# Kernel tuning notes

Hardware: AMD Instinct MI355X
Metric: run time of the kernel (lower is better)

## Reference

```python
import jax, jax.numpy as jnp
import numpy as np

D, H, DH, L, F, NM = 512, 8, 64, 8, 2048, 80
B, S = 8, 1024


def _ln(x, g, b, eps=1e-5):
    mu = x.mean(-1, keepdims=True)
    var = ((x - mu) ** 2).mean(-1, keepdims=True)
    return (x - mu) / jnp.sqrt(var + eps) * g + b


def setup_inputs() -> dict:
    key = jax.random.key(0)
    ks = jax.random.split(key, 16)
    n = lambda k, sh: jax.random.normal(k, sh, dtype=jnp.float32) * 0.02
    # sinusoidal positional encoding, as in PositionalEncoding
    pos = np.arange(S, dtype=np.float32)[:, None]
    div = np.exp(np.arange(0, D, 2, dtype=np.float32) * (-np.log(10000.0) / D))
    pe = np.zeros((S, D), dtype=np.float32)
    pe[:, 0::2] = np.sin(pos * div)
    pe[:, 1::2] = np.cos(pos * div)
    return dict(
        mel=jax.random.normal(ks[0], (B, S, NM), dtype=jnp.float32),
        pe=jnp.asarray(pe),
        proj_w=n(ks[1], (NM, D)), proj_b=jnp.zeros((D,), jnp.float32),
        Wq=n(ks[2], (L, D, D)), bq=jnp.zeros((L, D), jnp.float32),
        Wk=n(ks[3], (L, D, D)), bk=jnp.zeros((L, D), jnp.float32),
        Wv=n(ks[4], (L, D, D)), bv=jnp.zeros((L, D), jnp.float32),
        Wo=n(ks[5], (L, D, D)), bo=jnp.zeros((L, D), jnp.float32),
        ln1_g=jnp.ones((L, D), jnp.float32), ln1_b=jnp.zeros((L, D), jnp.float32),
        ln2_g=jnp.ones((L, D), jnp.float32), ln2_b=jnp.zeros((L, D), jnp.float32),
        Wi=n(ks[6], (L, D, F)), bi=jnp.zeros((L, F), jnp.float32),
        Wf=n(ks[7], (L, F, D)), bf=jnp.zeros((L, D), jnp.float32),
        lnf_g=jnp.ones((D,), jnp.float32), lnf_b=jnp.zeros((D,), jnp.float32),
        lang_w=n(ks[8], (D, 100)), lang_b=jnp.zeros((100,), jnp.float32),
        int_w=n(ks[9], (D, 50)), int_b=jnp.zeros((50,), jnp.float32),
        emo_w=n(ks[10], (D, 8)), emo_b=jnp.zeros((8,), jnp.float32),
        sp_w=n(ks[11], (D, 1000)), sp_b=jnp.zeros((1000,), jnp.float32),
    )


def reference(mel, pe, proj_w, proj_b, Wq, bq, Wk, bk, Wv, bv, Wo, bo,
              ln1_g, ln1_b, ln2_g, ln2_b, Wi, bi, Wf, bf,
              lnf_g, lnf_b, lang_w, lang_b, int_w, int_b, emo_w, emo_b, sp_w, sp_b):
    # feature extraction projection + positional encoding
    h = mel @ proj_w + proj_b + pe[None]  # (B, S, D)
    scale = 1.0 / np.sqrt(DH)

    def block(h, p):
        wq, bq_, wk, bk_, wv, bv_, wo, bo_, g1, b1, g2, b2, wi, bi_, wf, bf_ = p
        x = _ln(h, g1, b1)
        b, s, _ = x.shape
        heads = lambda y, w, bias: (y @ w + bias).reshape(b, s, H, DH).transpose(0, 2, 1, 3)
        q, k, v = heads(x, wq, bq_), heads(x, wk, bk_), heads(x, wv, bv_)
        probs = jax.nn.softmax(jnp.einsum('bhqd,bhkd->bhqk', q, k) * scale, axis=-1)
        ctx = jnp.einsum('bhqk,bhkd->bhqd', probs, v).transpose(0, 2, 1, 3).reshape(b, s, D)
        h = h + ctx @ wo + bo_
        y = _ln(h, g2, b2)
        h = h + jax.nn.gelu(y @ wi + bi_, approximate=False) @ wf + bf_
        return h, None

    h, _ = jax.lax.scan(block, h, (Wq, bq, Wk, bk, Wv, bv, Wo, bo,
                                   ln1_g, ln1_b, ln2_g, ln2_b, Wi, bi, Wf, bf))
    h = _ln(h, lnf_g, lnf_b)
    pooled = h.mean(axis=1)  # no mask: sequence_lengths=None path
    language_logits = pooled @ lang_w + lang_b
    intent_logits = pooled @ int_w + int_b
    emotion_logits = pooled @ emo_w + emo_b
    speech_logits = h @ sp_w + sp_b
    return (language_logits, intent_logits, emotion_logits, speech_logits)
```

## Files before the change

### kernel.cpp

```cpp
#include <hip/hip_runtime.h>
#include <hip/hip_bf16.h>
#include <math.h>

#define DD   512
#define HH   8
#define DHH  64
#define LL   8
#define FF   2048
#define NMEL 80
#define BB   8
#define SS   1024
#define MM   (BB*SS)

typedef __attribute__((ext_vector_type(8))) short bf16x8;
typedef __attribute__((ext_vector_type(4))) float f32x4;
typedef __attribute__((ext_vector_type(4))) unsigned short u16x4;

#define GLOAD_LDS16(g, l) __builtin_amdgcn_global_load_lds( \
    (const __attribute__((address_space(1))) void*)(g),      \
    (__attribute__((address_space(3))) void*)(l), 16, 0, 0)

__device__ __forceinline__ unsigned short f2bf(float x) {
    __hip_bfloat16 b = __float2bfloat16(x);
    return *reinterpret_cast<unsigned short*>(&b);
}

__global__ __launch_bounds__(256) void proj_pe_kernel(
    const float* __restrict__ mel, const float* __restrict__ pw,
    const float* __restrict__ pb, const float* __restrict__ pe,
    float* __restrict__ h)
{
    int row = blockIdx.x;
    int s = row & (SS - 1);
    __shared__ float m_s[NMEL];
    int t = threadIdx.x;
    if (t < NMEL) m_s[t] = mel[(size_t)row * NMEL + t];
    __syncthreads();
    for (int d = t; d < DD; d += 256) {
        float acc = pb[d] + pe[(size_t)s * DD + d];
        #pragma unroll 8
        for (int k = 0; k < NMEL; ++k)
            acc = fmaf(m_s[k], pw[(size_t)k * DD + d], acc);
        h[(size_t)row * DD + d] = acc;
    }
}

__global__ __launch_bounds__(256) void ln_kernel(
    const float* __restrict__ in, const float* __restrict__ g,
    const float* __restrict__ bta, __hip_bfloat16* __restrict__ out)
{
    int row = blockIdx.x;
    const float* xr = in + (size_t)row * DD;
    int t = threadIdx.x;
    float x0 = xr[t], x1 = xr[t + 256];
    float s = x0 + x1;
    float ss = x0 * x0 + x1 * x1;
    #pragma unroll
    for (int off = 32; off; off >>= 1) {
        s  += __shfl_down(s, off);
        ss += __shfl_down(ss, off);
    }
    __shared__ float red1[4], red2[4];
    int lane = t & 63, w = t >> 6;
    if (lane == 0) { red1[w] = s; red2[w] = ss; }
    __syncthreads();
    s  = red1[0] + red1[1] + red1[2] + red1[3];
    ss = red2[0] + red2[1] + red2[2] + red2[3];
    float mu  = s * (1.f / DD);
    float var = ss * (1.f / DD) - mu * mu;
    float rstd = rsqrtf(var + 1e-5f);
    out[(size_t)row * DD + t]       = __float2bfloat16((x0 - mu) * rstd * g[t]       + bta[t]);
    out[(size_t)row * DD + t + 256] = __float2bfloat16((x1 - mu) * rstd * g[t + 256] + bta[t + 256]);
}

__global__ __launch_bounds__(256) void wconv_kernel(
    const float* __restrict__ in, __hip_bfloat16* __restrict__ out,
    int K, int N, int rstride, int rowoff)
{
    __shared__ float tile[32][33];
    size_t lin  = (size_t)blockIdx.z * K * N;
    size_t lout = (size_t)blockIdx.z * rstride * K + (size_t)rowoff * K;
    int tx = threadIdx.x & 31, ty = threadIdx.x >> 5;
    int n0 = blockIdx.x * 32, k0 = blockIdx.y * 32;
    #pragma unroll
    for (int i = 0; i < 32; i += 8) {
        int k = k0 + ty + i, n = n0 + tx;
        tile[ty + i][tx] = (n < N) ? in[lin + (size_t)k * N + n] : 0.f;
    }
    __syncthreads();
    #pragma unroll
    for (int i = 0; i < 32; i += 8) {
        int n = n0 + ty + i, k = k0 + tx;
        out[lout + (size_t)n * K + k] = __float2bfloat16(tile[tx][ty + i]);
    }
}

template<int OUTMODE, bool GELU_EP, bool RESID>
__global__ __launch_bounds__(512) void gemm_bf16(
    const __hip_bfloat16* __restrict__ A,
    const __hip_bfloat16* __restrict__ Bt,
    const float* __restrict__ b0, const float* __restrict__ b1,
    const float* __restrict__ b2,
    const float* __restrict__ resid,
    float* __restrict__ Cf,
    __hip_bfloat16* __restrict__ O0, __hip_bfloat16* __restrict__ O1,
    __hip_bfloat16* __restrict__ O2,
    int M, int N, int K)
{
    __shared__ __align__(16) __hip_bfloat16 As[128 * 64];
    __shared__ __align__(16) __hip_bfloat16 Bs[128 * 64];
    int t = threadIdx.x;
    int w = t >> 6, lane = t & 63, g = lane >> 4, li = lane & 15;
    int wm = w >> 2, wn = w & 3;
    size_t bm = (size_t)blockIdx.y * 128;
    size_t bn = (size_t)blockIdx.x * 128;

    const f32x4 vzero = {0.f, 0.f, 0.f, 0.f};
    f32x4 acc[4][2];
    #pragma unroll
    for (int i = 0; i < 4; ++i)
        #pragma unroll
        for (int j = 0; j < 2; ++j) acc[i][j] = vzero;

    for (int k0 = 0; k0 < K; k0 += 64) {
        #pragma unroll
        for (int i = 0; i < 2; ++i) {
            int c = i * 512 + t;
            int row = c >> 3, col = (c & 7) << 3;
            GLOAD_LDS16(A + (bm + row) * (size_t)K + k0 + col, As + (size_t)c * 8);
        }
        #pragma unroll
        for (int i = 0; i < 2; ++i) {
            int c = i * 512 + t;
            int row = c >> 3, col = (c & 7) << 3;
            GLOAD_LDS16(Bt + (bn + row) * (size_t)K + k0 + col, Bs + (size_t)c * 8);
        }
        __syncthreads();
        #pragma unroll
        for (int kk = 0; kk < 2; ++kk) {
            bf16x8 af[4], bfr[2];
            #pragma unroll
            for (int mi = 0; mi < 4; ++mi)
                af[mi] = *reinterpret_cast<const bf16x8*>(As + (wm * 64 + mi * 16 + li) * 64 + kk * 32 + g * 8);
            #pragma unroll
            for (int ni = 0; ni < 2; ++ni)
                bfr[ni] = *reinterpret_cast<const bf16x8*>(Bs + (wn * 32 + ni * 16 + li) * 64 + kk * 32 + g * 8);
            #pragma unroll
            for (int mi = 0; mi < 4; ++mi)
                #pragma unroll
                for (int ni = 0; ni < 2; ++ni)
                    acc[mi][ni] = __builtin_amdgcn_mfma_f32_16x16x32_bf16(af[mi], bfr[ni], acc[mi][ni], 0, 0, 0);
        }
        __syncthreads();
    }

    #pragma unroll
    for (int mi = 0; mi < 4; ++mi) {
        #pragma unroll
        for (int ni = 0; ni < 2; ++ni) {
            f32x4 v = acc[mi][ni];
            int coll = wn * 32 + ni * 16 + li;
            size_t col = bn + coll;
            if ((int)col >= N) continue;
            float bv;
            int sel = 0, c = (int)col;
            if (OUTMODE == 2) {
                sel = (int)(col >> 9); c = (int)(col & 511);
                bv = (sel == 0) ? b0[c] : (sel == 1) ? b1[c] : b2[c];
            } else {
                bv = b0[col];
            }
            #pragma unroll
            for (int r = 0; r < 4; ++r) {
                size_t row = bm + wm * 64 + mi * 16 + g * 4 + r;
                float x = v[r] + bv;
                if (GELU_EP) x = 0.5f * x * (1.f + erff(x * 0.70710678118654752440f));
                if (RESID)   x += resid[row * (size_t)N + col];
                if (OUTMODE == 0) {
                    Cf[row * (size_t)N + col] = x;
                } else if (OUTMODE == 1) {
                    O0[row * (size_t)N + col] = __float2bfloat16(x);
                } else {
                    size_t b = row >> 10, s = row & (SS - 1);
                    size_t h = (size_t)(c >> 6), d = (size_t)(c & 63);
                    __hip_bfloat16 xb = __float2bfloat16(x);
                    if (sel == 0)      O0[((b * HH + h) << 16) + (s << 6) + d] = xb;
                    else if (sel == 1) O1[((b * HH + h) << 16) + (s << 6) + d] = xb;
                    else               O2[((b * HH + h) << 16) + (d << 10) + s] = xb;
                }
            }
        }
    }
}

__global__ __launch_bounds__(512, 4) void attn_mfma(
    const __hip_bfloat16* __restrict__ qb,
    const __hip_bfloat16* __restrict__ kb,
    const __hip_bfloat16* __restrict__ vtb,
    __hip_bfloat16* __restrict__ ctx)
{
    __shared__ __align__(16) char smem[49152];
    unsigned short (*Plds)[32][40] = (unsigned short (*)[32][40])smem;
    float* comb = (float*)smem;

    int t = threadIdx.x;
    int w = t >> 6, lane = t & 63, g = lane >> 4, li = lane & 15;
    int wq = w & 3, wk = w >> 2;
    int bh = blockIdx.y;
    int b = bh >> 3, h = bh & 7;
    int q0 = blockIdx.x * 128 + wq * 32;

    const __hip_bfloat16* Qp = qb  + ((size_t)bh << 16);
    const __hip_bfloat16* Kp = kb  + ((size_t)bh << 16);
    const __hip_bfloat16* Vp = vtb + ((size_t)bh << 16);

    bf16x8 qf[2][2];
    #pragma unroll
    for (int qt = 0; qt < 2; ++qt)
        #pragma unroll
        for (int kk = 0; kk < 2; ++kk)
            qf[qt][kk] = *reinterpret_cast<const bf16x8*>(
                Qp + (size_t)(q0 + qt * 16 + li) * DHH + kk * 32 + g * 8);

    const f32x4 vzero = {0.f, 0.f, 0.f, 0.f};
    f32x4 acc_oT[2][4];
    float m_r[2], l_r[2];
    #pragma unroll
    for (int qt = 0; qt < 2; ++qt) {
        #pragma unroll
        for (int dt = 0; dt < 4; ++dt) acc_oT[qt][dt] = vzero;
        m_r[qt] = -1e30f; l_r[qt] = 0.f;
    }

    const float csc = 0.125f * 1.44269504088896340736f;

    for (int it = 0; it < 16; ++it) {
        int ks0 = wk * 512 + it * 32;
        f32x4 accs[2][2];
        #pragma unroll
        for (int qt = 0; qt < 2; ++qt)
            #pragma unroll
            for (int kt = 0; kt < 2; ++kt) accs[qt][kt] = vzero;
        #pragma unroll
        for (int kk = 0; kk < 2; ++kk) {
            bf16x8 kf[2];
            #pragma unroll
            for (int kt = 0; kt < 2; ++kt)
                kf[kt] = *reinterpret_cast<const bf16x8*>(
                    Kp + (size_t)(ks0 + kt * 16 + li) * DHH + kk * 32 + g * 8);
            #pragma unroll
            for (int qt = 0; qt < 2; ++qt)
                #pragma unroll
                for (int kt = 0; kt < 2; ++kt)
                    accs[qt][kt] = __builtin_amdgcn_mfma_f32_16x16x32_bf16(kf[kt], qf[qt][kk], accs[qt][kt], 0, 0, 0);
        }

        float mnew[2];
        #pragma unroll
        for (int qt = 0; qt < 2; ++qt) {
            float a0 = fmaxf(fmaxf(accs[qt][0][0], accs[qt][0][1]),
                             fmaxf(accs[qt][0][2], accs[qt][0][3]));
            float a1 = fmaxf(fmaxf(accs[qt][1][0], accs[qt][1][1]),
                             fmaxf(accs[qt][1][2], accs[qt][1][3]));
            float m = fmaxf(a0, a1);
            m = fmaxf(m, __shfl_xor(m, 16));
            m = fmaxf(m, __shfl_xor(m, 32));
            mnew[qt] = m * csc;
        }

        bool grow = (mnew[0] > m_r[0] + 11.0f) || (mnew[1] > m_r[1] + 11.0f);
        if (__any(grow)) {
            #pragma unroll
            for (int qt = 0; qt < 2; ++qt) {
                float mn = fmaxf(m_r[qt], mnew[qt]);
                float alpha = exp2f(m_r[qt] - mn);
                m_r[qt] = mn;
                l_r[qt] *= alpha;
                #pragma unroll
                for (int dt = 0; dt < 4; ++dt)
                    #pragma unroll
                    for (int r = 0; r < 4; ++r)
                        acc_oT[qt][dt][r] *= alpha;
            }
        }

        float rs[2] = {0.f, 0.f};
        #pragma unroll
        for (int qt = 0; qt < 2; ++qt) {
            #pragma unroll
            for (int kt = 0; kt < 2; ++kt) {
                u16x4 pk;
                #pragma unroll
                for (int r = 0; r < 4; ++r) {
                    float p = exp2f(fmaf(accs[qt][kt][r], csc, -m_r[qt]));
                    rs[qt] += p;
                    pk[r] = f2bf(p);
                }
                *reinterpret_cast<u16x4*>(&Plds[w][qt * 16 + li][kt * 16 + g * 4]) = pk;
            }
            float s = rs[qt];
            s += __shfl_xor(s, 16);
            s += __shfl_xor(s, 32);
            l_r[qt] += s;
        }

        __builtin_amdgcn_wave_barrier();

        bf16x8 pf[2];
        #pragma unroll
        for (int qt = 0; qt < 2; ++qt)
            pf[qt] = *reinterpret_cast<const bf16x8*>(&Plds[w][qt * 16 + li][g * 8]);
        #pragma unroll
        for (int dt = 0; dt < 4; ++dt) {
            bf16x8 vf = *reinterpret_cast<const bf16x8*>(
                Vp + (size_t)(dt * 16 + li) * SS + ks0 + g * 8);
            #pragma unroll
            for (int qt = 0; qt < 2; ++qt)
                acc_oT[qt][dt] = __builtin_amdgcn_mfma_f32_16x16x32_bf16(vf, pf[qt], acc_oT[qt][dt], 0, 0, 0);
        }
        __builtin_amdgcn_wave_barrier();
    }

    __syncthreads();
    if (wk == 1) {
        float* cb = comb + ((size_t)(w - 4) * 64 + lane) * 36;
        #pragma unroll
        for (int qt = 0; qt < 2; ++qt)
            #pragma unroll
            for (int dt = 0; dt < 4; ++dt)
                *reinterpret_cast<f32x4*>(cb + qt * 16 + dt * 4) = acc_oT[qt][dt];
        #pragma unroll
        for (int qt = 0; qt < 2; ++qt) {
            cb[32 + qt] = m_r[qt];
            cb[34 + qt] = l_r[qt];
        }
    }
    __syncthreads();
    if (wk == 0) {
        float* cb = comb + ((size_t)w * 64 + lane) * 36;
        #pragma unroll
        for (int qt = 0; qt < 2; ++qt) {
            float m2 = cb[32 + qt];
            float l2 = cb[34 + qt];
            float mg = fmaxf(m_r[qt], m2);
            float a1 = exp2f(m_r[qt] - mg);
            float a2 = exp2f(m2 - mg);
            float inv = 1.f / (l_r[qt] * a1 + l2 * a2);
            int q = q0 + qt * 16 + li;
            #pragma unroll
            for (int dt = 0; dt < 4; ++dt) {
                f32x4 ob = *reinterpret_cast<const f32x4*>(cb + qt * 16 + dt * 4);
                u16x4 pk;
                #pragma unroll
                for (int r = 0; r < 4; ++r)
                    pk[r] = f2bf((acc_oT[qt][dt][r] * a1 + ob[r] * a2) * inv);
                *reinterpret_cast<u16x4*>(
                    &ctx[((size_t)(b * SS + q)) * DD + h * DHH + dt * 16 + g * 4]) = pk;
            }
        }
    }
}

__global__ __launch_bounds__(512) void pool_kernel(
    const __hip_bfloat16* __restrict__ hf, float* __restrict__ pooled)
{
    int b = blockIdx.x;
    int d = threadIdx.x;
    float acc = 0.f;
    for (int s = 0; s < SS; ++s)
        acc += __bfloat162float(hf[((size_t)(b * SS + s)) * DD + d]);
    pooled[b * DD + d] = acc * (1.f / SS);
}

__global__ __launch_bounds__(256) void heads_kernel(
    const float* __restrict__ pooled,
    const float* __restrict__ lw, const float* __restrict__ lb,
    const float* __restrict__ iw, const float* __restrict__ ib,
    const float* __restrict__ ew, const float* __restrict__ eb,
    float* __restrict__ out)
{
    int b = blockIdx.x;
    __shared__ float ps[DD];
    int t = threadIdx.x;
    ps[t] = pooled[b * DD + t];
    ps[t + 256] = pooled[b * DD + t + 256];
    __syncthreads();
    if (t < 158) {
        const float* wptr; const float* bptr; float* optr; int n; int j;
        if (t < 100)      { j = t;       wptr = lw; bptr = lb; optr = out;        n = 100; }
        else if (t < 150) { j = t - 100; wptr = iw; bptr = ib; optr = out + 800;  n = 50;  }
        else              { j = t - 150; wptr = ew; bptr = eb; optr = out + 1200; n = 8;   }
        float acc = bptr[j];
        for (int k2 = 0; k2 < DD; ++k2)
            acc = fmaf(ps[k2], wptr[(size_t)k2 * n + j], acc);
        optr[b * n + j] = acc;
    }
}

extern "C" void kernel_launch(void* const* d_in, const int* in_sizes, int n_in,
                              void* d_out, int out_size, void* d_ws, size_t ws_size,
                              hipStream_t stream)
{
    const float* mel    = (const float*)d_in[0];
    const float* pe     = (const float*)d_in[1];
    const float* proj_w = (const float*)d_in[2];
    const float* proj_b = (const float*)d_in[3];
    const float* Wq     = (const float*)d_in[4];
    const float* bq     = (const float*)d_in[5];
    const float* Wk     = (const float*)d_in[6];
    const float* bk     = (const float*)d_in[7];
    const float* Wv     = (const float*)d_in[8];
    const float* bv     = (const float*)d_in[9];
    const float* Wo     = (const float*)d_in[10];
    const float* bo     = (const float*)d_in[11];
    const float* ln1_g  = (const float*)d_in[12];
    const float* ln1_b  = (const float*)d_in[13];
    const float* ln2_g  = (const float*)d_in[14];
    const float* ln2_b  = (const float*)d_in[15];
    const float* Wi     = (const float*)d_in[16];
    const float* bi     = (const float*)d_in[17];
    const float* Wf     = (const float*)d_in[18];
    const float* bf     = (const float*)d_in[19];
    const float* lnf_g  = (const float*)d_in[20];
    const float* lnf_b  = (const float*)d_in[21];
    const float* lang_w = (const float*)d_in[22];
    const float* lang_b = (const float*)d_in[23];
    const float* int_w  = (const float*)d_in[24];
    const float* int_b  = (const float*)d_in[25];
    const float* emo_w  = (const float*)d_in[26];
    const float* emo_b  = (const float*)d_in[27];
    const float* sp_w   = (const float*)d_in[28];
    const float* sp_b   = (const float*)d_in[29];

    float* out = (float*)d_out;
    char* wsb = (char*)d_ws;

    const size_t MB = 1ull << 20;
    float* hbuf           = (float*)(wsb);
    __hip_bfloat16* xb    = (__hip_bfloat16*)(wsb + 16 * MB);
    __hip_bfloat16* qbuf  = (__hip_bfloat16*)(wsb + 24 * MB);
    __hip_bfloat16* kbuf  = (__hip_bfloat16*)(wsb + 32 * MB);
    __hip_bfloat16* vtb   = (__hip_bfloat16*)(wsb + 40 * MB);
    __hip_bfloat16* ctx   = (__hip_bfloat16*)(wsb + 48 * MB);
    __hip_bfloat16* gbuf  = (__hip_bfloat16*)(wsb + 24 * MB);
    float* pooled         = (float*)(wsb + 56 * MB);
    __hip_bfloat16* wqkv  = (__hip_bfloat16*)(wsb + 57 * MB);
    __hip_bfloat16* wot   = (__hip_bfloat16*)(wsb + 70 * MB);
    __hip_bfloat16* wit   = (__hip_bfloat16*)(wsb + 74 * MB);
    __hip_bfloat16* wft   = (__hip_bfloat16*)(wsb + 90 * MB);
    __hip_bfloat16* spt   = (__hip_bfloat16*)(wsb + 107 * MB);

    wconv_kernel<<<dim3(16, 16, LL), 256, 0, stream>>>(Wq, wqkv, DD, DD, 1536, 0);
    wconv_kernel<<<dim3(16, 16, LL), 256, 0, stream>>>(Wk, wqkv, DD, DD, 1536, 512);
    wconv_kernel<<<dim3(16, 16, LL), 256, 0, stream>>>(Wv, wqkv, DD, DD, 1536, 1024);
    wconv_kernel<<<dim3(16, 16, LL), 256, 0, stream>>>(Wo, wot, DD, DD, DD, 0);
    wconv_kernel<<<dim3(64, 16, LL), 256, 0, stream>>>(Wi, wit, DD, FF, FF, 0);
    wconv_kernel<<<dim3(16, 64, LL), 256, 0, stream>>>(Wf, wft, FF, DD, DD, 0);
    wconv_kernel<<<dim3(32, 16, 1),  256, 0, stream>>>(sp_w, spt, DD, 1000, 1024, 0);

    proj_pe_kernel<<<MM, 256, 0, stream>>>(mel, proj_w, proj_b, pe, hbuf);

    dim3 g512(4, 64);

    for (int l = 0; l < LL; ++l) {
        const __hip_bfloat16* wqkv_l = wqkv + (size_t)l * 1536 * DD;
        const __hip_bfloat16* wot_l  = wot  + (size_t)l * DD * DD;
        const __hip_bfloat16* wit_l  = wit  + (size_t)l * FF * DD;
        const __hip_bfloat16* wft_l  = wft  + (size_t)l * DD * FF;

        ln_kernel<<<MM, 256, 0, stream>>>(hbuf, ln1_g + l * DD, ln1_b + l * DD, xb);

        gemm_bf16<2, false, false><<<dim3(12, 64), 512, 0, stream>>>(
            xb, wqkv_l, bq + l * DD, bk + l * DD, bv + l * DD,
            nullptr, nullptr, qbuf, kbuf, vtb, MM, 1536, DD);

        attn_mfma<<<dim3(SS / 128, BB * HH), 512, 0, stream>>>(qbuf, kbuf, vtb, ctx);

        gemm_bf16<0, false, true><<<g512, 512, 0, stream>>>(
            ctx, wot_l, bo + l * DD, nullptr, nullptr,
            hbuf, hbuf, nullptr, nullptr, nullptr, MM, DD, DD);

        ln_kernel<<<MM, 256, 0, stream>>>(hbuf, ln2_g + l * DD, ln2_b + l * DD, xb);

        gemm_bf16<1, true, false><<<dim3(16, 64), 512, 0, stream>>>(
            xb, wit_l, bi + l * FF, nullptr, nullptr,
            nullptr, nullptr, gbuf, nullptr, nullptr, MM, FF, DD);
        gemm_bf16<0, false, true><<<g512, 512, 0, stream>>>(
            gbuf, wft_l, bf + l * DD, nullptr, nullptr,
            hbuf, hbuf, nullptr, nullptr, nullptr, MM, DD, FF);
    }

    ln_kernel<<<MM, 256, 0, stream>>>(hbuf, lnf_g, lnf_b, xb);
    pool_kernel<<<BB, 512, 0, stream>>>(xb, pooled);
    heads_kernel<<<BB, 256, 0, stream>>>(pooled, lang_w, lang_b, int_w, int_b,
                                         emo_w, emo_b, out);

    gemm_bf16<0, false, false><<<dim3(8, 64), 512, 0, stream>>>(
        xb, spt, sp_b, nullptr, nullptr,
        nullptr, out + 1264, nullptr, nullptr, nullptr, MM, 1000, DD);
}
```

Measured before the change: 1.885 ms.

## Use wave-per-row vectorized LayerNorm and 4-way key-split attention with larger key tiles

LayerNorm now processes one row per wavefront, eight rows per block, with float4 loads, xor-shuffle reductions and 16-byte bf16 stores, replacing the block-wide LDS reduction and barrier. The attention kernel now splits keys across four waves per query group (64 queries per block instead of 128) and processes 64 keys per iteration. That doubles the blocks and gives more MFMA work per softmax step. Partial results are merged in a two-level tree through shared memory, which adds extra barriers and LDS traffic at the end. The grid is also transposed so that heads vary fastest.

```diff
diff --git a/kernel.cpp b/kernel.cpp
--- a/kernel.cpp
+++ b/kernel.cpp
@@ -15,6 +15,7 @@
 typedef __attribute__((ext_vector_type(8))) short bf16x8;
 typedef __attribute__((ext_vector_type(4))) float f32x4;
 typedef __attribute__((ext_vector_type(4))) unsigned short u16x4;
+typedef __attribute__((ext_vector_type(8))) unsigned short u16x8;
 
 #define GLOAD_LDS16(g, l) __builtin_amdgcn_global_load_lds( \
     (const __attribute__((address_space(1))) void*)(g),      \
@@ -45,32 +46,38 @@
     }
 }
 
-__global__ __launch_bounds__(256) void ln_kernel(
+__global__ __launch_bounds__(512) void ln_kernel(
     const float* __restrict__ in, const float* __restrict__ g,
     const float* __restrict__ bta, __hip_bfloat16* __restrict__ out)
 {
-    int row = blockIdx.x;
-    const float* xr = in + (size_t)row * DD;
-    int t = threadIdx.x;
-    float x0 = xr[t], x1 = xr[t + 256];
-    float s = x0 + x1;
-    float ss = x0 * x0 + x1 * x1;
-    #pragma unroll
-    for (int off = 32; off; off >>= 1) {
-        s  += __shfl_down(s, off);
-        ss += __shfl_down(ss, off);
-    }
-    __shared__ float red1[4], red2[4];
-    int lane = t & 63, w = t >> 6;
-    if (lane == 0) { red1[w] = s; red2[w] = ss; }
-    __syncthreads();
-    s  = red1[0] + red1[1] + red1[2] + red1[3];
-    ss = red2[0] + red2[1] + red2[2] + red2[3];
+    int w = threadIdx.x >> 6, lane = threadIdx.x & 63;
+    int row = blockIdx.x * 8 + w;
+    const float4* xr = reinterpret_cast<const float4*>(in + (size_t)row * DD) + lane * 2;
+    float4 v0 = xr[0], v1 = xr[1];
+    float s  = v0.x + v0.y + v0.z + v0.w + v1.x + v1.y + v1.z + v1.w;
+    float ss = v0.x*v0.x + v0.y*v0.y + v0.z*v0.z + v0.w*v0.w
+             + v1.x*v1.x + v1.y*v1.y + v1.z*v1.z + v1.w*v1.w;
+    #pragma unroll
+    for (int off = 1; off < 64; off <<= 1) {
+        s  += __shfl_xor(s, off);
+        ss += __shfl_xor(ss, off);
+    }
     float mu  = s * (1.f / DD);
     float var = ss * (1.f / DD) - mu * mu;
     float rstd = rsqrtf(var + 1e-5f);
-    out[(size_t)row * DD + t]       = __float2bfloat16((x0 - mu) * rstd * g[t]       + bta[t]);
-    out[(size_t)row * DD + t + 256] = __float2bfloat16((x1 - mu) * rstd * g[t + 256] + bta[t + 256]);
+    const float4* gp = reinterpret_cast<const float4*>(g) + lane * 2;
+    const float4* bp = reinterpret_cast<const float4*>(bta) + lane * 2;
+    float4 g0 = gp[0], g1 = gp[1], b0 = bp[0], b1 = bp[1];
+    u16x8 o;
+    o[0] = f2bf((v0.x - mu) * rstd * g0.x + b0.x);
+    o[1] = f2bf((v0.y - mu) * rstd * g0.y + b0.y);
+    o[2] = f2bf((v0.z - mu) * rstd * g0.z + b0.z);
+    o[3] = f2bf((v0.w - mu) * rstd * g0.w + b0.w);
+    o[4] = f2bf((v1.x - mu) * rstd * g1.x + b1.x);
+    o[5] = f2bf((v1.y - mu) * rstd * g1.y + b1.y);
+    o[6] = f2bf((v1.z - mu) * rstd * g1.z + b1.z);
+    o[7] = f2bf((v1.w - mu) * rstd * g1.w + b1.w);
+    *reinterpret_cast<u16x8*>(out + (size_t)row * DD + lane * 8) = o;
 }
 
 __global__ __launch_bounds__(256) void wconv_kernel(
@@ -199,16 +206,16 @@
     const __hip_bfloat16* __restrict__ vtb,
     __hip_bfloat16* __restrict__ ctx)
 {
-    __shared__ __align__(16) char smem[49152];
-    unsigned short (*Plds)[32][40] = (unsigned short (*)[32][40])smem;
+    __shared__ __align__(16) char smem[36864];
+    unsigned short (*Plds)[32][72] = (unsigned short (*)[32][72])smem;
     float* comb = (float*)smem;
 
     int t = threadIdx.x;
     int w = t >> 6, lane = t & 63, g = lane >> 4, li = lane & 15;
-    int wq = w & 3, wk = w >> 2;
-    int bh = blockIdx.y;
+    int wq = w & 1, wk = w >> 1;
+    int bh = blockIdx.x;
     int b = bh >> 3, h = bh & 7;
-    int q0 = blockIdx.x * 128 + wq * 32;
+    int q0 = blockIdx.y * 64 + wq * 32;
 
     const __hip_bfloat16* Qp = qb  + ((size_t)bh << 16);
     const __hip_bfloat16* Kp = kb  + ((size_t)bh << 16);
@@ -234,35 +241,39 @@
 
     const float csc = 0.125f * 1.44269504088896340736f;
 
-    for (int it = 0; it < 16; ++it) {
-        int ks0 = wk * 512 + it * 32;
-        f32x4 accs[2][2];
+    for (int it = 0; it < 4; ++it) {
+        int ks0 = wk * 256 + it * 64;
+        f32x4 accs[2][4];
         #pragma unroll
         for (int qt = 0; qt < 2; ++qt)
             #pragma unroll
-            for (int kt = 0; kt < 2; ++kt) accs[qt][kt] = vzero;
+            for (int kt = 0; kt < 4; ++kt) accs[qt][kt] = vzero;
         #pragma unroll
         for (int kk = 0; kk < 2; ++kk) {
-            bf16x8 kf[2];
-            #pragma unroll
-            for (int kt = 0; kt < 2; ++kt)
+            bf16x8 kf[4];
+            #pragma unroll
+            for (int kt = 0; kt < 4; ++kt)
                 kf[kt] = *reinterpret_cast<const bf16x8*>(
                     Kp + (size_t)(ks0 + kt * 16 + li) * DHH + kk * 32 + g * 8);
             #pragma unroll
             for (int qt = 0; qt < 2; ++qt)
                 #pragma unroll
-                for (int kt = 0; kt < 2; ++kt)
+                for (int kt = 0; kt < 4; ++kt)
                     accs[qt][kt] = __builtin_amdgcn_mfma_f32_16x16x32_bf16(kf[kt], qf[qt][kk], accs[qt][kt], 0, 0, 0);
         }
 
         float mnew[2];
         #pragma unroll
         for (int qt = 0; qt < 2; ++qt) {
-            float a0 = fmaxf(fmaxf(accs[qt][0][0], accs[qt][0][1]),
-                             fmaxf(accs[qt][0][2], accs[qt][0][3]));
-            float a1 = fmaxf(fmaxf(accs[qt][1][0], accs[qt][1][1]),
-                             fmaxf(accs[qt][1][2], accs[qt][1][3]));
-            float m = fmaxf(a0, a1);
+            float m01 = fmaxf(fmaxf(accs[qt][0][0], accs[qt][0][1]),
+                              fmaxf(accs[qt][0][2], accs[qt][0][3]));
+            float m23 = fmaxf(fmaxf(accs[qt][1][0], accs[qt][1][1]),
+                              fmaxf(accs[qt][1][2], accs[qt][1][3]));
+            float m45 = fmaxf(fmaxf(accs[qt][2][0], accs[qt][2][1]),
+                              fmaxf(accs[qt][2][2], accs[qt][2][3]));
+            float m67 = fmaxf(fmaxf(accs[qt][3][0], accs[qt][3][1]),
+                              fmaxf(accs[qt][3][2], accs[qt][3][3]));
+            float m = fmaxf(fmaxf(m01, m23), fmaxf(m45, m67));
             m = fmaxf(m, __shfl_xor(m, 16));
             m = fmaxf(m, __shfl_xor(m, 32));
             mnew[qt] = m * csc;
@@ -284,64 +295,98 @@
             }
         }
 
-        float rs[2] = {0.f, 0.f};
         #pragma unroll
         for (int qt = 0; qt < 2; ++qt) {
-            #pragma unroll
-            for (int kt = 0; kt < 2; ++kt) {
+            float rs = 0.f;
+            #pragma unroll
+            for (int kt = 0; kt < 4; ++kt) {
                 u16x4 pk;
                 #pragma unroll
                 for (int r = 0; r < 4; ++r) {
                     float p = exp2f(fmaf(accs[qt][kt][r], csc, -m_r[qt]));
-                    rs[qt] += p;
+                    rs += p;
                     pk[r] = f2bf(p);
                 }
                 *reinterpret_cast<u16x4*>(&Plds[w][qt * 16 + li][kt * 16 + g * 4]) = pk;
             }
-            float s = rs[qt];
-            s += __shfl_xor(s, 16);
-            s += __shfl_xor(s, 32);
-            l_r[qt] += s;
+            rs += __shfl_xor(rs, 16);
+            rs += __shfl_xor(rs, 32);
+            l_r[qt] += rs;
         }
 
         __builtin_amdgcn_wave_barrier();
 
-        bf16x8 pf[2];
+        bf16x8 pf[2][2];
         #pragma unroll
         for (int qt = 0; qt < 2; ++qt)
-            pf[qt] = *reinterpret_cast<const bf16x8*>(&Plds[w][qt * 16 + li][g * 8]);
-        #pragma unroll
-        for (int dt = 0; dt < 4; ++dt) {
-            bf16x8 vf = *reinterpret_cast<const bf16x8*>(
-                Vp + (size_t)(dt * 16 + li) * SS + ks0 + g * 8);
-            #pragma unroll
-            for (int qt = 0; qt < 2; ++qt)
-                acc_oT[qt][dt] = __builtin_amdgcn_mfma_f32_16x16x32_bf16(vf, pf[qt], acc_oT[qt][dt], 0, 0, 0);
+            #pragma unroll
+            for (int ks = 0; ks < 2; ++ks)
+                pf[qt][ks] = *reinterpret_cast<const bf16x8*>(
+                    &Plds[w][qt * 16 + li][ks * 32 + g * 8]);
+        #pragma unroll
+        for (int ks = 0; ks < 2; ++ks) {
+            #pragma unroll
+            for (int dt = 0; dt < 4; ++dt) {
+                bf16x8 vf = *reinterpret_cast<const bf16x8*>(
+                    Vp + (size_t)(dt * 16 + li) * SS + ks0 + ks * 32 + g * 8);
+                #pragma unroll
+                for (int qt = 0; qt < 2; ++qt)
+                    acc_oT[qt][dt] = __builtin_amdgcn_mfma_f32_16x16x32_bf16(vf, pf[qt][ks], acc_oT[qt][dt], 0, 0, 0);
+            }
         }
         __builtin_amdgcn_wave_barrier();
     }
 
     __syncthreads();
-    if (wk == 1) {
-        float* cb = comb + ((size_t)(w - 4) * 64 + lane) * 36;
+    if (wk & 1) {
+        int slot = wq + (wk >> 1) * 2;
+        float* cb = comb + ((size_t)slot * 64 + lane) * 36;
         #pragma unroll
         for (int qt = 0; qt < 2; ++qt)
             #pragma unroll
             for (int dt = 0; dt < 4; ++dt)
                 *reinterpret_cast<f32x4*>(cb + qt * 16 + dt * 4) = acc_oT[qt][dt];
+        cb[32] = m_r[0]; cb[33] = m_r[1];
+        cb[34] = l_r[0]; cb[35] = l_r[1];
+    }
+    __syncthreads();
+    if (!(wk & 1)) {
+        int slot = wq + wk;
+        float* cb = comb + ((size_t)slot * 64 + lane) * 36;
         #pragma unroll
         for (int qt = 0; qt < 2; ++qt) {
-            cb[32 + qt] = m_r[qt];
-            cb[34 + qt] = l_r[qt];
-        }
+            float m2 = cb[32 + qt], l2 = cb[34 + qt];
+            float mg = fmaxf(m_r[qt], m2);
+            float a1 = exp2f(m_r[qt] - mg);
+            float a2 = exp2f(m2 - mg);
+            m_r[qt] = mg;
+            l_r[qt] = l_r[qt] * a1 + l2 * a2;
+            #pragma unroll
+            for (int dt = 0; dt < 4; ++dt) {
+                f32x4 ob = *reinterpret_cast<const f32x4*>(cb + qt * 16 + dt * 4);
+                #pragma unroll
+                for (int r = 0; r < 4; ++r)
+                    acc_oT[qt][dt][r] = acc_oT[qt][dt][r] * a1 + ob[r] * a2;
+            }
+        }
+    }
+    __syncthreads();
+    if (wk == 2) {
+        float* cb = comb + ((size_t)wq * 64 + lane) * 36;
+        #pragma unroll
+        for (int qt = 0; qt < 2; ++qt)
+            #pragma unroll
+            for (int dt = 0; dt < 4; ++dt)
+                *reinterpret_cast<f32x4*>(cb + qt * 16 + dt * 4) = acc_oT[qt][dt];
+        cb[32] = m_r[0]; cb[33] = m_r[1];
+        cb[34] = l_r[0]; cb[35] = l_r[1];
     }
     __syncthreads();
     if (wk == 0) {
-        float* cb = comb + ((size_t)w * 64 + lane) * 36;
+        float* cb = comb + ((size_t)wq * 64 + lane) * 36;
         #pragma unroll
         for (int qt = 0; qt < 2; ++qt) {
-            float m2 = cb[32 + qt];
-            float l2 = cb[34 + qt];
+            float m2 = cb[32 + qt], l2 = cb[34 + qt];
             float mg = fmaxf(m_r[qt], m2);
             float a1 = exp2f(m_r[qt] - mg);
             float a2 = exp2f(m2 - mg);
@@ -468,19 +513,19 @@
         const __hip_bfloat16* wit_l  = wit  + (size_t)l * FF * DD;
         const __hip_bfloat16* wft_l  = wft  + (size_t)l * DD * FF;
 
-        ln_kernel<<<MM, 256, 0, stream>>>(hbuf, ln1_g + l * DD, ln1_b + l * DD, xb);
+        ln_kernel<<<MM / 8, 512, 0, stream>>>(hbuf, ln1_g + l * DD, ln1_b + l * DD, xb);
 
         gemm_bf16<2, false, false><<<dim3(12, 64), 512, 0, stream>>>(
             xb, wqkv_l, bq + l * DD, bk + l * DD, bv + l * DD,
             nullptr, nullptr, qbuf, kbuf, vtb, MM, 1536, DD);
 
-        attn_mfma<<<dim3(SS / 128, BB * HH), 512, 0, stream>>>(qbuf, kbuf, vtb, ctx);
+        attn_mfma<<<dim3(BB * HH, SS / 64), 512, 0, stream>>>(qbuf, kbuf, vtb, ctx);
 
         gemm_bf16<0, false, true><<<g512, 512, 0, stream>>>(
             ctx, wot_l, bo + l * DD, nullptr, nullptr,
             hbuf, hbuf, nullptr, nullptr, nullptr, MM, DD, DD);
 
-        ln_kernel<<<MM, 256, 0, stream>>>(hbuf, ln2_g + l * DD, ln2_b + l * DD, xb);
+        ln_kernel<<<MM / 8, 512, 0, stream>>>(hbuf, ln2_g + l * DD, ln2_b + l * DD, xb);
 
         gemm_bf16<1, true, false><<<dim3(16, 64), 512, 0, stream>>>(
             xb, wit_l, bi + l * FF, nullptr, nullptr,
@@ -490,7 +535,7 @@
             hbuf, hbuf, nullptr, nullptr, nullptr, MM, DD, FF);
     }
 
-    ln_kernel<<<MM, 256, 0, stream>>>(hbuf, lnf_g, lnf_b, xb);
+    ln_kernel<<<MM / 8, 512, 0, stream>>>(hbuf, lnf_g, lnf_b, xb);
     pool_kernel<<<BB, 512, 0, stream>>>(xb, pooled);
     heads_kernel<<<BB, 256, 0, stream>>>(pooled, lang_w, lang_b, int_w, int_b,
                                          emo_w, emo_b, out);
```

Result: slower. 1.998 ms (+6.0%).
